# Optimization experiments

Measured on AMD Instinct MI355X. Metric: run time of the kernel, lower is better.

The kernel has to match this reference:

```python
import jax, jax.numpy as jnp
import numpy as np

N_NODES = 50000
N_EDGES = 1_600_000


def add_self_loops(edge_index, n):
    loops = jnp.arange(n, dtype=edge_index.dtype)
    return jnp.concatenate([edge_index, jnp.stack([loops, loops])], axis=1)


def gat_layer(x, edge_index, W, a_src, a_dst, b):
    """PyG GATConv (concat=True, negative_slope=0.2, add_self_loops handled by caller)."""
    src, dst = edge_index[0], edge_index[1]
    n = x.shape[0]
    H, C = a_src.shape
    xp = (x @ W).reshape(n, H, C)                       # [N,H,C] transformed features
    al_src = jnp.einsum('nhc,hc->nh', xp, a_src)        # [N,H]
    al_dst = jnp.einsum('nhc,hc->nh', xp, a_dst)        # [N,H]
    logits = jax.nn.leaky_relu(al_src[src] + al_dst[dst], negative_slope=0.2)  # [E,H]
    m = jax.lax.stop_gradient(jax.ops.segment_max(logits, dst, num_segments=n))
    e = jnp.exp(logits - m[dst])                        # stable segment softmax
    denom = jax.ops.segment_sum(e, dst, num_segments=n)
    alpha = e / denom[dst]                              # [E,H]
    out = jax.ops.segment_sum(xp[src] * alpha[:, :, None], dst, num_segments=n)  # [N,H,C]
    return out.reshape(n, H * C) + b


def setup_inputs() -> dict:
    key = jax.random.key(0)
    ks = jax.random.split(key, 11)
    s = 0.1  # weight scale
    return {
        'x': jax.random.normal(ks[0], (N_NODES, 128), jnp.float32),
        'edge_index': jax.random.randint(ks[1], (2, N_EDGES), 0, N_NODES, jnp.int32),
        'W1': s * jax.random.normal(ks[2], (128, 128), jnp.float32),
        'a_src1': s * jax.random.normal(ks[3], (2, 64), jnp.float32),
        'a_dst1': s * jax.random.normal(ks[4], (2, 64), jnp.float32),
        'b1': s * jax.random.normal(ks[5], (128,), jnp.float32),
        'W2': s * jax.random.normal(ks[6], (128, 64), jnp.float32),
        'a_src2': s * jax.random.normal(ks[7], (2, 32), jnp.float32),
        'a_dst2': s * jax.random.normal(ks[8], (2, 32), jnp.float32),
        'b2': s * jax.random.normal(ks[9], (64,), jnp.float32),
    }


def reference(x, edge_index, W1, a_src1, a_dst1, b1, W2, a_src2, a_dst2, b2):
    ei = add_self_loops(edge_index, x.shape[0])
    encoded = x  # FeatureEncoding with no auxiliary features: identity passthrough
    h = jax.nn.elu(gat_layer(encoded, ei, W1, a_src1, a_dst1, b1))
    out = jax.nn.elu(gat_layer(h, ei, W2, a_src2, a_dst2, b2))
    return (out, encoded)
```

## Files before the change

kernel.cpp:

```cpp
#include <hip/hip_runtime.h>
#include <math.h>

#define N_NODES 50000
#define N_EDGES 1600000
#define EA (N_EDGES + N_NODES)
#define MAXD 128
#define NBUCK 196
#define EPB 4096
#define BCAP 16000

typedef unsigned int uint32;
typedef float f32x4 __attribute__((ext_vector_type(4)));
typedef _Float16 h16x2 __attribute__((ext_vector_type(2)));
typedef _Float16 f16x8 __attribute__((ext_vector_type(8)));

__device__ inline h16x2 u2h(uint32 u) { return __builtin_bit_cast(h16x2, u); }
__device__ inline uint32 h2u(h16x2 h) { return __builtin_bit_cast(uint32, h); }
__device__ inline uint32 pkh(float a, float b) {
  return __builtin_bit_cast(uint32, __builtin_amdgcn_cvt_pkrtz(a, b));
}
__device__ inline ushort f2h(float f) {
  _Float16 h = (_Float16)f;
  return __builtin_bit_cast(ushort, h);
}
__device__ inline int clampi(int v, int lo, int hi) {
  return v < lo ? lo : (v > hi ? hi : v);
}

template<int N, bool AF16, bool COPYX>
__global__ __launch_bounds__(256) void gemm_mfma_kernel(
    const void* __restrict__ Ap, const float* __restrict__ B,
    const float* __restrict__ asrc, const float* __restrict__ adst,
    ushort* __restrict__ Cb, float* __restrict__ al, float* __restrict__ encout, int M) {
  constexpr int KK = 4;
  constexpr int NC = N / 16;
  __shared__ uint32 Bl[KK * NC * 64 * 4];
  const int t = threadIdx.x;

  for (int id = t; id < KK * NC * 64; id += 256) {
    int lane = id & 63;
    int cf = (id >> 6) % NC;
    int kk = (id >> 6) / NC;
    int col = cf * 16 + (lane & 15);
    int k0 = kk * 32 + (lane >> 4) * 8;
    uint32 w0 = pkh(B[(k0 + 0) * N + col], B[(k0 + 1) * N + col]);
    uint32 w1 = pkh(B[(k0 + 2) * N + col], B[(k0 + 3) * N + col]);
    uint32 w2 = pkh(B[(k0 + 4) * N + col], B[(k0 + 5) * N + col]);
    uint32 w3 = pkh(B[(k0 + 6) * N + col], B[(k0 + 7) * N + col]);
    *reinterpret_cast<uint4*>(&Bl[id * 4]) = make_uint4(w0, w1, w2, w3);
  }
  __syncthreads();

  const int w = t >> 6, lane = t & 63;
  const int l15 = lane & 15, g4 = lane >> 4;
  const int row0 = blockIdx.x * 64 + w * 16;
  int arow = row0 + l15; if (arow > M - 1) arow = M - 1;
  const int k0 = g4 * 8;

  f32x4 acc[NC];
#pragma unroll
  for (int c = 0; c < NC; ++c) acc[c] = f32x4{0.f, 0.f, 0.f, 0.f};

#pragma unroll
  for (int kk = 0; kk < KK; ++kk) {
    f16x8 af;
    if (AF16) {
      af = *reinterpret_cast<const f16x8*>((const ushort*)Ap + (size_t)arow * 128 + kk * 32 + k0);
    } else {
      const float* A = (const float*)Ap;
      float4 a0 = *reinterpret_cast<const float4*>(A + (size_t)arow * 128 + kk * 32 + k0);
      float4 a1 = *reinterpret_cast<const float4*>(A + (size_t)arow * 128 + kk * 32 + k0 + 4);
      if (COPYX) {
        *reinterpret_cast<float4*>(encout + (size_t)arow * 128 + kk * 32 + k0)     = a0;
        *reinterpret_cast<float4*>(encout + (size_t)arow * 128 + kk * 32 + k0 + 4) = a1;
      }
      union { uint32 u[4]; f16x8 v; } p;
      p.u[0] = pkh(a0.x, a0.y);
      p.u[1] = pkh(a0.z, a0.w);
      p.u[2] = pkh(a1.x, a1.y);
      p.u[3] = pkh(a1.z, a1.w);
      af = p.v;
    }
#pragma unroll
    for (int c = 0; c < NC; ++c) {
      f16x8 bf = *reinterpret_cast<const f16x8*>(&Bl[((kk * NC + c) * 64 + lane) * 4]);
      acc[c] = __builtin_amdgcn_mfma_f32_16x16x32_f16(af, bf, acc[c], 0, 0, 0);
    }
  }

  float as_c[NC], ad_c[NC];
#pragma unroll
  for (int c = 0; c < NC; ++c) { as_c[c] = asrc[c * 16 + l15]; ad_c[c] = adst[c * 16 + l15]; }
#pragma unroll
  for (int reg = 0; reg < 4; ++reg) {
    int row = row0 + g4 * 4 + reg;
    bool ok = row < M;
    float ps0 = 0.f, ps1 = 0.f, pd0 = 0.f, pd1 = 0.f;
#pragma unroll
    for (int c = 0; c < NC; ++c) {
      float v = acc[c][reg];
      if (ok) Cb[(size_t)row * N + c * 16 + l15] = f2h(v);
      if (c < NC / 2) { ps0 += v * as_c[c]; pd0 += v * ad_c[c]; }
      else            { ps1 += v * as_c[c]; pd1 += v * ad_c[c]; }
    }
#pragma unroll
    for (int off = 8; off >= 1; off >>= 1) {
      ps0 += __shfl_xor(ps0, off); ps1 += __shfl_xor(ps1, off);
      pd0 += __shfl_xor(pd0, off); pd1 += __shfl_xor(pd1, off);
    }
    if (ok && l15 == 0)
      *reinterpret_cast<float4*>(&al[row * 4]) = make_float4(ps0, ps1, pd0, pd1);
  }
}

__global__ void init_bcur_kernel(int* __restrict__ bcur) {
  int b = blockIdx.x * blockDim.x + threadIdx.x;
  if (b < NBUCK) bcur[b] = b * BCAP;
}

__global__ void partA_kernel(const int* __restrict__ src, const int* __restrict__ dst,
                             int* __restrict__ bcur, uint32* __restrict__ ebuf) {
  __shared__ int h[NBUCK];
  __shared__ int lo[NBUCK];
  __shared__ int rank_[NBUCK];
  __shared__ int gbase[NBUCK];
  __shared__ uint32 staged[EPB];
  const int t = threadIdx.x;
  const int e0 = blockIdx.x * EPB;
  const int ne = min(EPB, N_EDGES - e0);

  for (int i = t; i < NBUCK; i += 256) h[i] = 0;
  __syncthreads();
  for (int i = t; i < ne; i += 256) {
    int d = dst[e0 + i];
    atomicAdd(&h[d >> 8], 1);
  }
  __syncthreads();
  if (t == 0) {
    int a = 0;
    for (int b = 0; b < NBUCK; ++b) { lo[b] = a; a += h[b]; }
  }
  __syncthreads();
  for (int i = t; i < NBUCK; i += 256) rank_[i] = lo[i];
  __syncthreads();
  for (int i = t; i < ne; i += 256) {
    int d = dst[e0 + i];
    int s = src[e0 + i];
    int b = d >> 8;
    int r = atomicAdd(&rank_[b], 1);
    staged[r] = ((uint32)b << 24) | ((uint32)s << 8) | (uint32)(d & 255);
  }
  __syncthreads();
  if (t < NBUCK) gbase[t] = atomicAdd(&bcur[t], h[t]);
  __syncthreads();
  if (t < NBUCK) rank_[t] = gbase[t] - lo[t];
  __syncthreads();
  for (int i = t; i < ne; i += 256) {
    uint32 wd = staged[i];
    ebuf[rank_[wd >> 24] + i] = wd;
  }
}

__global__ void scan196_kernel(const int* __restrict__ bcur, int* __restrict__ bbase,
                               int* __restrict__ row_start) {
  __shared__ int wsh[4];
  const int t = threadIdx.x, lane = t & 63, wv = t >> 6;
  int v = 0;
  if (t < NBUCK) {
    int nn = min(256, N_NODES - t * 256);
    v = (bcur[t] - t * BCAP) + nn;
  }
  int x = v;
  for (int off = 1; off < 64; off <<= 1) {
    int y = __shfl_up(x, off);
    if (lane >= off) x += y;
  }
  if (lane == 63) wsh[wv] = x;
  __syncthreads();
  int wo = 0;
  for (int w = 0; w < wv; ++w) wo += wsh[w];
  if (t < NBUCK) bbase[t] = wo + x - v;
  if (t == 0) row_start[N_NODES] = EA;
}

__global__ __launch_bounds__(256) void partB2_kernel(
    const int* __restrict__ bcur, const int* __restrict__ bbase,
    const uint32* __restrict__ ebuf, int* __restrict__ row_start,
    int* __restrict__ sorted_src) {
  __shared__ uint32 sl[BCAP];
  __shared__ int h[256];
  __shared__ int cur[256];
  __shared__ int wsh[4];
  const int b = blockIdx.x;
  const int t = threadIdx.x, lane = t & 63, wv = t >> 6;
  h[t] = 0;
  __syncthreads();
  const int base = b * BCAP;
  const int len = min(bcur[b] - base, BCAP);
  for (int i = t; i < len; i += 256) {
    uint32 w = ebuf[base + i];
    sl[i] = w;
    atomicAdd(&h[w & 255], 1);
  }
  __syncthreads();
  const int n = b * 256 + t;
  const bool valid = n < N_NODES;
  int v = valid ? h[t] + 1 : 0;
  int x = v;
  for (int off = 1; off < 64; off <<= 1) {
    int y = __shfl_up(x, off);
    if (lane >= off) x += y;
  }
  if (lane == 63) wsh[wv] = x;
  __syncthreads();
  int wo = 0;
  for (int w = 0; w < wv; ++w) wo += wsh[w];
  int rs = bbase[b] + wo + x - v;
  if (valid) {
    row_start[n] = rs;
    sorted_src[rs] = n;
    cur[t] = rs + 1;
  }
  __syncthreads();
  for (int i = t; i < len; i += 256) {
    uint32 w = sl[i];
    int pos = atomicAdd(&cur[w & 255], 1);
    sorted_src[pos] = (int)((w >> 8) & 0xffffu);
  }
}

template<int HC, bool OUTF16>
__global__ __launch_bounds__(256) void agg_kernel(
    const ushort* __restrict__ xh, const float* __restrict__ al,
    const int* __restrict__ row_start, const int* __restrict__ sorted_src,
    const float* __restrict__ bias, void* __restrict__ outp) {
  __shared__ uint2 pL[4][2][MAXD];
  const int wid = (blockIdx.x * blockDim.x + threadIdx.x) >> 6;
  const int lane = threadIdx.x & 63;
  const int wv = (threadIdx.x >> 6) & 3;
  if (wid >= N_NODES) return;
  const float4* al4 = (const float4*)al;
  const uint32* xb32 = (const uint32*)xh;
  int start = row_start[wid], end = row_start[wid + 1];
  start = clampi(start, 0, EA);
  end   = clampi(end, start, EA);
  const int deg = end - start;
  float4 mya = al4[wid];
  const float ad0 = mya.z, ad1 = mya.w;
  const float ESH = 2.7725887f;

  float m0 = -1e30f, m1 = -1e30f, d0 = 0.f, d1 = 0.f;

  if (deg > MAXD) {
    for (int i = start + lane; i < end; i += 64) {
      int s = clampi(sorted_src[i], 0, N_NODES - 1);
      float4 a = al4[s];
      float l0 = a.x + ad0; l0 = l0 > 0.f ? l0 : 0.2f * l0;
      float l1 = a.y + ad1; l1 = l1 > 0.f ? l1 : 0.2f * l1;
      m0 = fmaxf(m0, l0); m1 = fmaxf(m1, l1);
    }
    for (int off = 32; off >= 1; off >>= 1) {
      m0 = fmaxf(m0, __shfl_xor(m0, off));
      m1 = fmaxf(m1, __shfl_xor(m1, off));
    }
    for (int i = start + lane; i < end; i += 64) {
      int s = clampi(sorted_src[i], 0, N_NODES - 1);
      float4 a = al4[s];
      float l0 = a.x + ad0; l0 = l0 > 0.f ? l0 : 0.2f * l0;
      float l1 = a.y + ad1; l1 = l1 > 0.f ? l1 : 0.2f * l1;
      d0 += __expf(l0 - m0); d1 += __expf(l1 - m1);
    }
    for (int off = 32; off >= 1; off >>= 1) {
      d0 += __shfl_xor(d0, off);
      d1 += __shfl_xor(d1, off);
    }
    const float inv0 = 1.f / d0, inv1 = 1.f / d1;
    constexpr int AL = HC / 2;
    const int cols0 = lane * 2;
    const int head = cols0 >= HC / 2;
    const float invh = head ? inv1 : inv0;
    const float mh = head ? m1 : m0;
    const float adh = head ? ad1 : ad0;
    float a0 = 0.f, a1 = 0.f;
    if (lane < AL) {
      for (int i = start; i < end; ++i) {
        int s = clampi(sorted_src[i], 0, N_NODES - 1);
        float lv = al[s * 4 + head] + adh;
        lv = lv > 0.f ? lv : 0.2f * lv;
        float wgt = __expf(lv - mh) * invh;
        h16x2 hx = u2h(xb32[(size_t)s * AL + lane]);
        a0 = fmaf(wgt, (float)hx[0], a0);
        a1 = fmaf(wgt, (float)hx[1], a1);
      }
      float o0 = a0 + bias[cols0];
      float o1 = a1 + bias[cols0 + 1];
      o0 = o0 > 0.f ? o0 : __expf(o0) - 1.f;
      o1 = o1 > 0.f ? o1 : __expf(o1) - 1.f;
      if (OUTF16) ((uint32*)outp)[(size_t)wid * AL + lane] = pkh(o0, o1);
      else *reinterpret_cast<float2*>((float*)outp + (size_t)wid * HC + cols0) = make_float2(o0, o1);
    }
    return;
  }

  constexpr int LPR = HC / 8;
  constexpr int EPI = 64 / LPR;
  constexpr int RS  = HC / 2;
  constexpr int PF  = 4;
  const int q  = lane / LPR;
  const int cc = lane % LPR;
  const int hd = cc / (LPR / 2);
  const uint2* myP = &pL[wv][hd][0];
  const uint32* myx = xb32 + cc * 4;

  for (int i = start + lane; i < end; i += 64) {
    int s = clampi(sorted_src[i], 0, N_NODES - 1);
    float4 a = al4[s];
    float l0 = a.x + ad0; l0 = l0 > 0.f ? l0 : 0.2f * l0;
    float l1 = a.y + ad1; l1 = l1 > 0.f ? l1 : 0.2f * l1;
    float e0 = __expf(l0 - ESH);
    float e1 = __expf(l1 - ESH);
    int j = i - start;
    pL[wv][0][j] = make_uint2((uint32)s, pkh(e0, e0));
    pL[wv][1][j] = make_uint2((uint32)s, pkh(e1, e1));
    d0 += e0; d1 += e1;
  }

  uint4 pv[PF];
  h16x2 pw[PF];
#pragma unroll
  for (int st = 0; st < PF; ++st) {
    int jj = st * EPI + q;
    int jc = jj < deg ? jj : 0;
    uint2 p = myP[jc];
    pw[st] = u2h(jj < deg ? p.y : 0u);
    pv[st] = *reinterpret_cast<const uint4*>(myx + (size_t)p.x * RS);
  }

  for (int off = 32; off >= 1; off >>= 1) {
    d0 += __shfl_xor(d0, off);
    d1 += __shfl_xor(d1, off);
  }
  const float inv0 = 1.f / d0, inv1 = 1.f / d1;

  h16x2 acc2[4];
#pragma unroll
  for (int k = 0; k < 4; ++k) acc2[k] = u2h(0u);

#pragma unroll
  for (int st = 0; st < PF; ++st) {
    acc2[0] += pw[st] * u2h(pv[st].x); acc2[1] += pw[st] * u2h(pv[st].y);
    acc2[2] += pw[st] * u2h(pv[st].z); acc2[3] += pw[st] * u2h(pv[st].w);
  }

  int j = PF * EPI;
  for (; j + 4 * EPI <= deg; j += 4 * EPI) {
    uint2 p0 = myP[j + q];
    uint2 p1 = myP[j + EPI + q];
    uint2 p2 = myP[j + 2 * EPI + q];
    uint2 p3 = myP[j + 3 * EPI + q];
    const uint4 v0 = *reinterpret_cast<const uint4*>(myx + (size_t)p0.x * RS);
    const uint4 v1 = *reinterpret_cast<const uint4*>(myx + (size_t)p1.x * RS);
    const uint4 v2 = *reinterpret_cast<const uint4*>(myx + (size_t)p2.x * RS);
    const uint4 v3 = *reinterpret_cast<const uint4*>(myx + (size_t)p3.x * RS);
    h16x2 w0 = u2h(p0.y), w1 = u2h(p1.y), w2 = u2h(p2.y), w3 = u2h(p3.y);
    acc2[0] += w0 * u2h(v0.x); acc2[1] += w0 * u2h(v0.y);
    acc2[2] += w0 * u2h(v0.z); acc2[3] += w0 * u2h(v0.w);
    acc2[0] += w1 * u2h(v1.x); acc2[1] += w1 * u2h(v1.y);
    acc2[2] += w1 * u2h(v1.z); acc2[3] += w1 * u2h(v1.w);
    acc2[0] += w2 * u2h(v2.x); acc2[1] += w2 * u2h(v2.y);
    acc2[2] += w2 * u2h(v2.z); acc2[3] += w2 * u2h(v2.w);
    acc2[0] += w3 * u2h(v3.x); acc2[1] += w3 * u2h(v3.y);
    acc2[2] += w3 * u2h(v3.z); acc2[3] += w3 * u2h(v3.w);
  }
  for (; j + EPI <= deg; j += EPI) {
    uint2 p = myP[j + q];
    h16x2 w2 = u2h(p.y);
    const uint4 v = *reinterpret_cast<const uint4*>(myx + (size_t)p.x * RS);
    acc2[0] += w2 * u2h(v.x); acc2[1] += w2 * u2h(v.y);
    acc2[2] += w2 * u2h(v.z); acc2[3] += w2 * u2h(v.w);
  }
  if (j < deg) {
    int jj = j + q;
    int jc = jj < deg ? jj : 0;
    uint2 p = myP[jc];
    h16x2 w2 = u2h(jj < deg ? p.y : 0u);
    const uint4 v = *reinterpret_cast<const uint4*>(myx + (size_t)p.x * RS);
    acc2[0] += w2 * u2h(v.x); acc2[1] += w2 * u2h(v.y);
    acc2[2] += w2 * u2h(v.z); acc2[3] += w2 * u2h(v.w);
  }

#pragma unroll
  for (int k = 0; k < 4; ++k) {
    if (LPR == 8) acc2[k] = u2h((uint32)__shfl_xor((int)h2u(acc2[k]), 8)) + acc2[k];
    acc2[k] = u2h((uint32)__shfl_xor((int)h2u(acc2[k]), 16)) + acc2[k];
    acc2[k] = u2h((uint32)__shfl_xor((int)h2u(acc2[k]), 32)) + acc2[k];
  }

  if (q == 0) {
    const float invh = hd ? inv1 : inv0;
    float o[8];
#pragma unroll
    for (int k = 0; k < 4; ++k) {
      o[2 * k]     = (float)acc2[k][0] * invh + bias[cc * 8 + 2 * k];
      o[2 * k + 1] = (float)acc2[k][1] * invh + bias[cc * 8 + 2 * k + 1];
    }
#pragma unroll
    for (int k = 0; k < 8; ++k) o[k] = o[k] > 0.f ? o[k] : __expf(o[k]) - 1.f;
    if (OUTF16) {
      uint4 u;
      u.x = pkh(o[0], o[1]); u.y = pkh(o[2], o[3]);
      u.z = pkh(o[4], o[5]); u.w = pkh(o[6], o[7]);
      *reinterpret_cast<uint4*>((uint32*)outp + (size_t)wid * RS + cc * 4) = u;
    } else {
      float* op = (float*)outp + (size_t)wid * HC + cc * 8;
      *reinterpret_cast<float4*>(op)     = make_float4(o[0], o[1], o[2], o[3]);
      *reinterpret_cast<float4*>(op + 4) = make_float4(o[4], o[5], o[6], o[7]);
    }
  }
}

extern "C" void kernel_launch(void* const* d_in, const int* in_sizes, int n_in,
                              void* d_out, int out_size, void* d_ws, size_t ws_size,
                              hipStream_t stream) {
  const float* x      = (const float*)d_in[0];
  const int*   ei     = (const int*)d_in[1];
  const float* W1     = (const float*)d_in[2];
  const float* a_src1 = (const float*)d_in[3];
  const float* a_dst1 = (const float*)d_in[4];
  const float* b1     = (const float*)d_in[5];
  const float* W2     = (const float*)d_in[6];
  const float* a_src2 = (const float*)d_in[7];
  const float* a_dst2 = (const float*)d_in[8];
  const float* b2     = (const float*)d_in[9];
  float* out = (float*)d_out;

  char* ws = (char*)d_ws;
  size_t off = 0;
  auto alloc = [&](size_t bytes) {
    void* p = ws + off;
    off = (off + bytes + 255) & ~(size_t)255;
    return p;
  };
  ushort* xh1       = (ushort*)alloc((size_t)N_NODES * 128 * 2);
  ushort* h1h       = (ushort*)alloc((size_t)N_NODES * 128 * 2);
  ushort* xh2       = (ushort*)alloc((size_t)N_NODES * 64 * 2);
  float*  al1       = (float*)alloc((size_t)N_NODES * 4 * 4);
  float*  al2       = (float*)alloc((size_t)N_NODES * 4 * 4);
  int*    row_start = (int*)alloc((size_t)(N_NODES + 1) * 4);
  int*    bbase     = (int*)alloc(256 * 4);
  int*    bcur      = (int*)alloc(NBUCK * 4);
  int*    sorted_src= (int*)alloc((size_t)EA * 4);
  uint32* ebuf      = (uint32*)h1h;

  const int* src = ei;
  const int* dst = ei + N_EDGES;

  const int waveBlocks = (N_NODES * 64) / 256;
  const int partBlocks = (N_EDGES + EPB - 1) / EPB;
  const int gemmBlocks = (N_NODES + 63) / 64;

  init_bcur_kernel<<<1, 256, 0, stream>>>(bcur);
  partA_kernel<<<partBlocks, 256, 0, stream>>>(src, dst, bcur, ebuf);
  scan196_kernel<<<1, 256, 0, stream>>>(bcur, bbase, row_start);
  partB2_kernel<<<NBUCK, 256, 0, stream>>>(bcur, bbase, ebuf, row_start, sorted_src);

  gemm_mfma_kernel<128, false, true><<<gemmBlocks, 256, 0, stream>>>(
      x, W1, a_src1, a_dst1, xh1, al1, out + (size_t)N_NODES * 64, N_NODES);
  agg_kernel<128, true><<<waveBlocks, 256, 0, stream>>>(xh1, al1, row_start, sorted_src, b1, h1h);

  gemm_mfma_kernel<64, true, false><<<gemmBlocks, 256, 0, stream>>>(
      h1h, W2, a_src2, a_dst2, xh2, al2, nullptr, N_NODES);
  agg_kernel<64, false><<<waveBlocks, 256, 0, stream>>>(xh2, al2, row_start, sorted_src, b2, out);
}
```

Baseline: 160.3 us.

## Split feature buffers per head and run one wave per node-head in aggregation

Transformed features and attention logits are now stored head-major, as two separate planes per layer. Aggregation launches one wave per (node, head) pair, so each wave gathers only half-width rows. That halves per-wave register and LDS state and doubles the number of waves. The bucket scan kernel and the bcur init kernel are removed: partB2 computes its base offset by reducing bcur, and a memset replaces the init. In exchange, sorted_src, row_start and the softmax logits are read twice per node, once per head, and the main gather loop unroll drops from 4 to 2.

```diff
diff --git a/kernel.cpp b/kernel.cpp
--- a/kernel.cpp
+++ b/kernel.cpp
@@ -34,6 +34,7 @@
     ushort* __restrict__ Cb, float* __restrict__ al, float* __restrict__ encout, int M) {
   constexpr int KK = 4;
   constexpr int NC = N / 16;
+  constexpr int NH = N / 2;
   __shared__ uint32 Bl[KK * NC * 64 * 4];
   const int t = threadIdx.x;
 
@@ -65,7 +66,10 @@
   for (int kk = 0; kk < KK; ++kk) {
     f16x8 af;
     if (AF16) {
-      af = *reinterpret_cast<const f16x8*>((const ushort*)Ap + (size_t)arow * 128 + kk * 32 + k0);
+      int kabs = kk * 32 + k0;
+      int kh = kabs >= 64;
+      af = *reinterpret_cast<const f16x8*>(
+          (const ushort*)Ap + (size_t)kh * N_NODES * 64 + (size_t)arow * 64 + (kabs - kh * 64));
     } else {
       const float* A = (const float*)Ap;
       float4 a0 = *reinterpret_cast<const float4*>(A + (size_t)arow * 128 + kk * 32 + k0);
@@ -99,7 +103,11 @@
 #pragma unroll
     for (int c = 0; c < NC; ++c) {
       float v = acc[c][reg];
-      if (ok) Cb[(size_t)row * N + c * 16 + l15] = f2h(v);
+      if (ok) {
+        int col = c * 16 + l15;
+        int ch = col >= NH;
+        Cb[(size_t)ch * N_NODES * NH + (size_t)row * NH + (col - ch * NH)] = f2h(v);
+      }
       if (c < NC / 2) { ps0 += v * as_c[c]; pd0 += v * ad_c[c]; }
       else            { ps1 += v * as_c[c]; pd1 += v * ad_c[c]; }
     }
@@ -108,14 +116,11 @@
       ps0 += __shfl_xor(ps0, off); ps1 += __shfl_xor(ps1, off);
       pd0 += __shfl_xor(pd0, off); pd1 += __shfl_xor(pd1, off);
     }
-    if (ok && l15 == 0)
-      *reinterpret_cast<float4*>(&al[row * 4]) = make_float4(ps0, ps1, pd0, pd1);
-  }
-}
-
-__global__ void init_bcur_kernel(int* __restrict__ bcur) {
-  int b = blockIdx.x * blockDim.x + threadIdx.x;
-  if (b < NBUCK) bcur[b] = b * BCAP;
+    if (ok && l15 == 0) {
+      ((float2*)al)[row]           = make_float2(ps0, pd0);
+      ((float2*)al)[N_NODES + row] = make_float2(ps1, pd1);
+    }
+  }
 }
 
 __global__ void partA_kernel(const int* __restrict__ src, const int* __restrict__ dst,
@@ -123,7 +128,6 @@
   __shared__ int h[NBUCK];
   __shared__ int lo[NBUCK];
   __shared__ int rank_[NBUCK];
-  __shared__ int gbase[NBUCK];
   __shared__ uint32 staged[EPB];
   const int t = threadIdx.x;
   const int e0 = blockIdx.x * EPB;
@@ -151,9 +155,10 @@
     staged[r] = ((uint32)b << 24) | ((uint32)s << 8) | (uint32)(d & 255);
   }
   __syncthreads();
-  if (t < NBUCK) gbase[t] = atomicAdd(&bcur[t], h[t]);
-  __syncthreads();
-  if (t < NBUCK) rank_[t] = gbase[t] - lo[t];
+  if (t < NBUCK) {
+    int old = atomicAdd(&bcur[t], h[t]);
+    rank_[t] = t * BCAP + old - lo[t];
+  }
   __syncthreads();
   for (int i = t; i < ne; i += 256) {
     uint32 wd = staged[i];
@@ -161,42 +166,25 @@
   }
 }
 
-__global__ void scan196_kernel(const int* __restrict__ bcur, int* __restrict__ bbase,
-                               int* __restrict__ row_start) {
-  __shared__ int wsh[4];
-  const int t = threadIdx.x, lane = t & 63, wv = t >> 6;
-  int v = 0;
-  if (t < NBUCK) {
-    int nn = min(256, N_NODES - t * 256);
-    v = (bcur[t] - t * BCAP) + nn;
-  }
-  int x = v;
-  for (int off = 1; off < 64; off <<= 1) {
-    int y = __shfl_up(x, off);
-    if (lane >= off) x += y;
-  }
-  if (lane == 63) wsh[wv] = x;
-  __syncthreads();
-  int wo = 0;
-  for (int w = 0; w < wv; ++w) wo += wsh[w];
-  if (t < NBUCK) bbase[t] = wo + x - v;
-  if (t == 0) row_start[N_NODES] = EA;
-}
-
 __global__ __launch_bounds__(256) void partB2_kernel(
-    const int* __restrict__ bcur, const int* __restrict__ bbase,
-    const uint32* __restrict__ ebuf, int* __restrict__ row_start,
-    int* __restrict__ sorted_src) {
+    const int* __restrict__ bcur, const uint32* __restrict__ ebuf,
+    int* __restrict__ row_start, int* __restrict__ sorted_src) {
   __shared__ uint32 sl[BCAP];
   __shared__ int h[256];
   __shared__ int cur[256];
   __shared__ int wsh[4];
+  __shared__ int red[4];
   const int b = blockIdx.x;
   const int t = threadIdx.x, lane = t & 63, wv = t >> 6;
+  int myv = 0;
+  if (t < b) myv = bcur[t] + min(256, N_NODES - t * 256);
+  for (int off = 32; off >= 1; off >>= 1) myv += __shfl_xor(myv, off);
+  if (lane == 0) red[wv] = myv;
   h[t] = 0;
   __syncthreads();
+  const int bbase = red[0] + red[1] + red[2] + red[3];
   const int base = b * BCAP;
-  const int len = min(bcur[b] - base, BCAP);
+  const int len = min(bcur[b], BCAP);
   for (int i = t; i < len; i += 256) {
     uint32 w = ebuf[base + i];
     sl[i] = w;
@@ -215,12 +203,13 @@
   __syncthreads();
   int wo = 0;
   for (int w = 0; w < wv; ++w) wo += wsh[w];
-  int rs = bbase[b] + wo + x - v;
+  int rs = bbase + wo + x - v;
   if (valid) {
     row_start[n] = rs;
     sorted_src[rs] = n;
     cur[t] = rs + 1;
   }
+  if (b == 0 && t == 0) row_start[N_NODES] = EA;
   __syncthreads();
   for (int i = t; i < len; i += 256) {
     uint32 w = sl[i];
@@ -229,101 +218,84 @@
   }
 }
 
-template<int HC, bool OUTF16>
+template<int HCH, bool OUTF16>
 __global__ __launch_bounds__(256) void agg_kernel(
     const ushort* __restrict__ xh, const float* __restrict__ al,
     const int* __restrict__ row_start, const int* __restrict__ sorted_src,
     const float* __restrict__ bias, void* __restrict__ outp) {
-  __shared__ uint2 pL[4][2][MAXD];
-  const int wid = (blockIdx.x * blockDim.x + threadIdx.x) >> 6;
+  constexpr int RSH = HCH / 2;
+  constexpr int LPR = HCH / 8;
+  constexpr int EPI = 64 / LPR;
+  constexpr int PF  = 32 / EPI;
+  __shared__ uint2 pL[4][MAXD];
+  const int gw = (blockIdx.x * blockDim.x + threadIdx.x) >> 6;
   const int lane = threadIdx.x & 63;
   const int wv = (threadIdx.x >> 6) & 3;
-  if (wid >= N_NODES) return;
-  const float4* al4 = (const float4*)al;
-  const uint32* xb32 = (const uint32*)xh;
-  int start = row_start[wid], end = row_start[wid + 1];
+  if (gw >= 2 * N_NODES) return;
+  const int head = gw >= N_NODES ? 1 : 0;
+  const int node = gw - head * N_NODES;
+  const float2* alh = (const float2*)al + (size_t)head * N_NODES;
+  const uint32* xb32 = (const uint32*)xh + (size_t)head * N_NODES * RSH;
+  int start = row_start[node], end = row_start[node + 1];
   start = clampi(start, 0, EA);
   end   = clampi(end, start, EA);
   const int deg = end - start;
-  float4 mya = al4[wid];
-  const float ad0 = mya.z, ad1 = mya.w;
+  const float adh = alh[node].y;
   const float ESH = 2.7725887f;
-
-  float m0 = -1e30f, m1 = -1e30f, d0 = 0.f, d1 = 0.f;
+  float dsum = 0.f;
 
   if (deg > MAXD) {
+    float m = -1e30f;
     for (int i = start + lane; i < end; i += 64) {
       int s = clampi(sorted_src[i], 0, N_NODES - 1);
-      float4 a = al4[s];
-      float l0 = a.x + ad0; l0 = l0 > 0.f ? l0 : 0.2f * l0;
-      float l1 = a.y + ad1; l1 = l1 > 0.f ? l1 : 0.2f * l1;
-      m0 = fmaxf(m0, l0); m1 = fmaxf(m1, l1);
-    }
-    for (int off = 32; off >= 1; off >>= 1) {
-      m0 = fmaxf(m0, __shfl_xor(m0, off));
-      m1 = fmaxf(m1, __shfl_xor(m1, off));
-    }
+      float l = alh[s].x + adh; l = l > 0.f ? l : 0.2f * l;
+      m = fmaxf(m, l);
+    }
+    for (int off = 32; off >= 1; off >>= 1) m = fmaxf(m, __shfl_xor(m, off));
     for (int i = start + lane; i < end; i += 64) {
       int s = clampi(sorted_src[i], 0, N_NODES - 1);
-      float4 a = al4[s];
-      float l0 = a.x + ad0; l0 = l0 > 0.f ? l0 : 0.2f * l0;
-      float l1 = a.y + ad1; l1 = l1 > 0.f ? l1 : 0.2f * l1;
-      d0 += __expf(l0 - m0); d1 += __expf(l1 - m1);
-    }
-    for (int off = 32; off >= 1; off >>= 1) {
-      d0 += __shfl_xor(d0, off);
-      d1 += __shfl_xor(d1, off);
-    }
-    const float inv0 = 1.f / d0, inv1 = 1.f / d1;
-    constexpr int AL = HC / 2;
-    const int cols0 = lane * 2;
-    const int head = cols0 >= HC / 2;
-    const float invh = head ? inv1 : inv0;
-    const float mh = head ? m1 : m0;
-    const float adh = head ? ad1 : ad0;
-    float a0 = 0.f, a1 = 0.f;
-    if (lane < AL) {
+      float l = alh[s].x + adh; l = l > 0.f ? l : 0.2f * l;
+      dsum += __expf(l - m);
+    }
+    for (int off = 32; off >= 1; off >>= 1) dsum += __shfl_xor(dsum, off);
+    const float inv = 1.f / dsum;
+    if (lane < RSH) {
+      float a0 = 0.f, a1 = 0.f;
       for (int i = start; i < end; ++i) {
         int s = clampi(sorted_src[i], 0, N_NODES - 1);
-        float lv = al[s * 4 + head] + adh;
-        lv = lv > 0.f ? lv : 0.2f * lv;
-        float wgt = __expf(lv - mh) * invh;
-        h16x2 hx = u2h(xb32[(size_t)s * AL + lane]);
-        a0 = fmaf(wgt, (float)hx[0], a0);
-        a1 = fmaf(wgt, (float)hx[1], a1);
+        float l = alh[s].x + adh; l = l > 0.f ? l : 0.2f * l;
+        float w = __expf(l - m) * inv;
+        h16x2 hx = u2h(xb32[(size_t)s * RSH + lane]);
+        a0 = fmaf(w, (float)hx[0], a0);
+        a1 = fmaf(w, (float)hx[1], a1);
       }
+      int cols0 = head * HCH + lane * 2;
       float o0 = a0 + bias[cols0];
       float o1 = a1 + bias[cols0 + 1];
       o0 = o0 > 0.f ? o0 : __expf(o0) - 1.f;
       o1 = o1 > 0.f ? o1 : __expf(o1) - 1.f;
-      if (OUTF16) ((uint32*)outp)[(size_t)wid * AL + lane] = pkh(o0, o1);
-      else *reinterpret_cast<float2*>((float*)outp + (size_t)wid * HC + cols0) = make_float2(o0, o1);
+      if (OUTF16) {
+        ((uint32*)outp)[(size_t)head * N_NODES * RSH + (size_t)node * RSH + lane] = pkh(o0, o1);
+      } else {
+        float* op = (float*)outp + (size_t)node * (2 * HCH) + head * HCH + lane * 2;
+        op[0] = o0; op[1] = o1;
+      }
     }
     return;
   }
 
-  constexpr int LPR = HC / 8;
-  constexpr int EPI = 64 / LPR;
-  constexpr int RS  = HC / 2;
-  constexpr int PF  = 4;
+  for (int i = start + lane; i < end; i += 64) {
+    int s = clampi(sorted_src[i], 0, N_NODES - 1);
+    float l = alh[s].x + adh; l = l > 0.f ? l : 0.2f * l;
+    float e = __expf(l - ESH);
+    pL[wv][i - start] = make_uint2((uint32)s, pkh(e, e));
+    dsum += e;
+  }
+
   const int q  = lane / LPR;
   const int cc = lane % LPR;
-  const int hd = cc / (LPR / 2);
-  const uint2* myP = &pL[wv][hd][0];
+  const uint2* myP = &pL[wv][0];
   const uint32* myx = xb32 + cc * 4;
-
-  for (int i = start + lane; i < end; i += 64) {
-    int s = clampi(sorted_src[i], 0, N_NODES - 1);
-    float4 a = al4[s];
-    float l0 = a.x + ad0; l0 = l0 > 0.f ? l0 : 0.2f * l0;
-    float l1 = a.y + ad1; l1 = l1 > 0.f ? l1 : 0.2f * l1;
-    float e0 = __expf(l0 - ESH);
-    float e1 = __expf(l1 - ESH);
-    int j = i - start;
-    pL[wv][0][j] = make_uint2((uint32)s, pkh(e0, e0));
-    pL[wv][1][j] = make_uint2((uint32)s, pkh(e1, e1));
-    d0 += e0; d1 += e1;
-  }
 
   uint4 pv[PF];
   h16x2 pw[PF];
@@ -333,14 +305,11 @@
     int jc = jj < deg ? jj : 0;
     uint2 p = myP[jc];
     pw[st] = u2h(jj < deg ? p.y : 0u);
-    pv[st] = *reinterpret_cast<const uint4*>(myx + (size_t)p.x * RS);
-  }
-
-  for (int off = 32; off >= 1; off >>= 1) {
-    d0 += __shfl_xor(d0, off);
-    d1 += __shfl_xor(d1, off);
-  }
-  const float inv0 = 1.f / d0, inv1 = 1.f / d1;
+    pv[st] = *reinterpret_cast<const uint4*>(myx + (size_t)p.x * RSH);
+  }
+
+  for (int off = 32; off >= 1; off >>= 1) dsum += __shfl_xor(dsum, off);
+  const float inv = 1.f / dsum;
 
   h16x2 acc2[4];
 #pragma unroll
@@ -353,56 +322,40 @@
   }
 
   int j = PF * EPI;
-  for (; j + 4 * EPI <= deg; j += 4 * EPI) {
+  for (; j + 2 * EPI <= deg; j += 2 * EPI) {
     uint2 p0 = myP[j + q];
     uint2 p1 = myP[j + EPI + q];
-    uint2 p2 = myP[j + 2 * EPI + q];
-    uint2 p3 = myP[j + 3 * EPI + q];
-    const uint4 v0 = *reinterpret_cast<const uint4*>(myx + (size_t)p0.x * RS);
-    const uint4 v1 = *reinterpret_cast<const uint4*>(myx + (size_t)p1.x * RS);
-    const uint4 v2 = *reinterpret_cast<const uint4*>(myx + (size_t)p2.x * RS);
-    const uint4 v3 = *reinterpret_cast<const uint4*>(myx + (size_t)p3.x * RS);
-    h16x2 w0 = u2h(p0.y), w1 = u2h(p1.y), w2 = u2h(p2.y), w3 = u2h(p3.y);
+    const uint4 v0 = *reinterpret_cast<const uint4*>(myx + (size_t)p0.x * RSH);
+    const uint4 v1 = *reinterpret_cast<const uint4*>(myx + (size_t)p1.x * RSH);
+    h16x2 w0 = u2h(p0.y), w1 = u2h(p1.y);
     acc2[0] += w0 * u2h(v0.x); acc2[1] += w0 * u2h(v0.y);
     acc2[2] += w0 * u2h(v0.z); acc2[3] += w0 * u2h(v0.w);
     acc2[0] += w1 * u2h(v1.x); acc2[1] += w1 * u2h(v1.y);
     acc2[2] += w1 * u2h(v1.z); acc2[3] += w1 * u2h(v1.w);
-    acc2[0] += w2 * u2h(v2.x); acc2[1] += w2 * u2h(v2.y);
-    acc2[2] += w2 * u2h(v2.z); acc2[3] += w2 * u2h(v2.w);
-    acc2[0] += w3 * u2h(v3.x); acc2[1] += w3 * u2h(v3.y);
-    acc2[2] += w3 * u2h(v3.z); acc2[3] += w3 * u2h(v3.w);
-  }
-  for (; j + EPI <= deg; j += EPI) {
-    uint2 p = myP[j + q];
-    h16x2 w2 = u2h(p.y);
-    const uint4 v = *reinterpret_cast<const uint4*>(myx + (size_t)p.x * RS);
-    acc2[0] += w2 * u2h(v.x); acc2[1] += w2 * u2h(v.y);
-    acc2[2] += w2 * u2h(v.z); acc2[3] += w2 * u2h(v.w);
-  }
-  if (j < deg) {
+  }
+  for (; j < deg; j += EPI) {
     int jj = j + q;
     int jc = jj < deg ? jj : 0;
     uint2 p = myP[jc];
     h16x2 w2 = u2h(jj < deg ? p.y : 0u);
-    const uint4 v = *reinterpret_cast<const uint4*>(myx + (size_t)p.x * RS);
+    const uint4 v = *reinterpret_cast<const uint4*>(myx + (size_t)p.x * RSH);
     acc2[0] += w2 * u2h(v.x); acc2[1] += w2 * u2h(v.y);
     acc2[2] += w2 * u2h(v.z); acc2[3] += w2 * u2h(v.w);
   }
 
 #pragma unroll
   for (int k = 0; k < 4; ++k) {
-    if (LPR == 8) acc2[k] = u2h((uint32)__shfl_xor((int)h2u(acc2[k]), 8)) + acc2[k];
-    acc2[k] = u2h((uint32)__shfl_xor((int)h2u(acc2[k]), 16)) + acc2[k];
-    acc2[k] = u2h((uint32)__shfl_xor((int)h2u(acc2[k]), 32)) + acc2[k];
+#pragma unroll
+    for (int off = LPR; off < 64; off <<= 1)
+      acc2[k] = u2h((uint32)__shfl_xor((int)h2u(acc2[k]), off)) + acc2[k];
   }
 
   if (q == 0) {
-    const float invh = hd ? inv1 : inv0;
     float o[8];
 #pragma unroll
     for (int k = 0; k < 4; ++k) {
-      o[2 * k]     = (float)acc2[k][0] * invh + bias[cc * 8 + 2 * k];
-      o[2 * k + 1] = (float)acc2[k][1] * invh + bias[cc * 8 + 2 * k + 1];
+      o[2 * k]     = (float)acc2[k][0] * inv + bias[head * HCH + cc * 8 + 2 * k];
+      o[2 * k + 1] = (float)acc2[k][1] * inv + bias[head * HCH + cc * 8 + 2 * k + 1];
     }
 #pragma unroll
     for (int k = 0; k < 8; ++k) o[k] = o[k] > 0.f ? o[k] : __expf(o[k]) - 1.f;
@@ -410,9 +363,10 @@
       uint4 u;
       u.x = pkh(o[0], o[1]); u.y = pkh(o[2], o[3]);
       u.z = pkh(o[4], o[5]); u.w = pkh(o[6], o[7]);
-      *reinterpret_cast<uint4*>((uint32*)outp + (size_t)wid * RS + cc * 4) = u;
+      *reinterpret_cast<uint4*>((uint32*)outp + (size_t)head * N_NODES * RSH +
+                                (size_t)node * RSH + cc * 4) = u;
     } else {
-      float* op = (float*)outp + (size_t)wid * HC + cc * 8;
+      float* op = (float*)outp + (size_t)node * (2 * HCH) + head * HCH + cc * 8;
       *reinterpret_cast<float4*>(op)     = make_float4(o[0], o[1], o[2], o[3]);
       *reinterpret_cast<float4*>(op + 4) = make_float4(o[4], o[5], o[6], o[7]);
     }
@@ -447,7 +401,6 @@
   float*  al1       = (float*)alloc((size_t)N_NODES * 4 * 4);
   float*  al2       = (float*)alloc((size_t)N_NODES * 4 * 4);
   int*    row_start = (int*)alloc((size_t)(N_NODES + 1) * 4);
-  int*    bbase     = (int*)alloc(256 * 4);
   int*    bcur      = (int*)alloc(NBUCK * 4);
   int*    sorted_src= (int*)alloc((size_t)EA * 4);
   uint32* ebuf      = (uint32*)h1h;
@@ -455,20 +408,19 @@
   const int* src = ei;
   const int* dst = ei + N_EDGES;
 
-  const int waveBlocks = (N_NODES * 64) / 256;
+  const int aggBlocks  = (2 * N_NODES * 64) / 256;
   const int partBlocks = (N_EDGES + EPB - 1) / EPB;
   const int gemmBlocks = (N_NODES + 63) / 64;
 
-  init_bcur_kernel<<<1, 256, 0, stream>>>(bcur);
+  hipMemsetAsync(bcur, 0, NBUCK * 4, stream);
   partA_kernel<<<partBlocks, 256, 0, stream>>>(src, dst, bcur, ebuf);
-  scan196_kernel<<<1, 256, 0, stream>>>(bcur, bbase, row_start);
-  partB2_kernel<<<NBUCK, 256, 0, stream>>>(bcur, bbase, ebuf, row_start, sorted_src);
+  partB2_kernel<<<NBUCK, 256, 0, stream>>>(bcur, ebuf, row_start, sorted_src);
 
   gemm_mfma_kernel<128, false, true><<<gemmBlocks, 256, 0, stream>>>(
       x, W1, a_src1, a_dst1, xh1, al1, out + (size_t)N_NODES * 64, N_NODES);
-  agg_kernel<128, true><<<waveBlocks, 256, 0, stream>>>(xh1, al1, row_start, sorted_src, b1, h1h);
+  agg_kernel<64, true><<<aggBlocks, 256, 0, stream>>>(xh1, al1, row_start, sorted_src, b1, h1h);
 
   gemm_mfma_kernel<64, true, false><<<gemmBlocks, 256, 0, stream>>>(
       h1h, W2, a_src2, a_dst2, xh2, al2, nullptr, N_NODES);
-  agg_kernel<64, false><<<waveBlocks, 256, 0, stream>>>(xh2, al2, row_start, sorted_src, b2, out);
-}
+  agg_kernel<32, false><<<aggBlocks, 256, 0, stream>>>(xh2, al2, row_start, sorted_src, b2, out);
+}
```

After: 168.7 us. 5.2% more time.
